# Kernel tuning notes

Measured on AMD Instinct MI355X. Metric: run time of the kernel, lower is better.

## Reference

```python
import jax, jax.numpy as jnp
import numpy as np

jax.config.update("jax_enable_x64", True)  # I-BERT's FixedPointMul runs in double precision

# I-BERT IntSoftmax constants
COEF0 = 0.35815147
COEF1 = 0.96963238 / COEF0
COEF2 = 1.0 / COEF0
X0 = -0.6931          # -ln(2)
N_EXP = 30            # large integer n in int_exp
MAX_BIT = 32
OUTPUT_BIT = 8
ACT_BIT = 16

B, H, S = 1, 12, 2048


def sg(x):
    return jax.lax.stop_gradient(x)


def ste_round(x):
    # straight-through round (matches torch round_ste / SymmetricQuantFunction backward)
    return x + sg(jnp.round(x) - x)


def ste_floor(x):
    return x + sg(jnp.floor(x) - x)


def sym_scale(x_min, x_max, bits):
    # symmetric_linear_quantization_params: scale = clamp(max(|min|,|max|),1e-8)/(2^(b-1)-1)
    n = 2 ** (bits - 1) - 1
    s = jnp.maximum(jnp.abs(x_min), jnp.abs(x_max))
    return sg(jnp.maximum(s, 1e-8) / n)


def fixedpoint_mul(pre_act, pre_sf, z_sf, bits):
    # I-BERT fixedpoint_mul: requantize pre_act (granularity pre_sf) to scale z_sf
    # using a 31-bit mantissa frexp decomposition, computed in float64.
    n = 2 ** (bits - 1) - 1
    z_int = ste_round(pre_act.astype(jnp.float64) / pre_sf.astype(jnp.float64))
    new_scale = sg((pre_sf / z_sf).astype(jnp.float64))
    e = jnp.floor(jnp.log2(jnp.abs(new_scale))) + 1.0   # frexp exponent
    m_int = jnp.round((new_scale / 2.0 ** e) * 2.0 ** 31)  # 31-bit mantissa
    out = ste_round(z_int * m_int / 2.0 ** (31.0 - e))
    return jnp.clip(out, -n - 1, n).astype(jnp.float32)


def quant_softmax(x):
    n16 = 2 ** (ACT_BIT - 1) - 1
    # ---- outer QuantAct(16, symmetric), specified min/max = data min/max ----
    sf = sym_scale(sg(x.min()), sg(x.max()), ACT_BIT)
    x_int = jnp.clip(ste_round(x / sf), -n16 - 1, n16)
    quant_x = x_int * sf  # dequantized activation returned by QuantAct
    # ---- IntSoftmax ----
    xi = quant_x / sf
    xi = xi - xi.max(axis=-1, keepdims=True)
    # int_exp: shift-based exponential, exp(x) = 2^(-q) * exp(r), r in (-ln2, 0]
    x0_int = sg(jnp.floor(X0 / sf))               # negative integer
    xi = jnp.maximum(xi, N_EXP * x0_int)
    q = ste_floor(xi / x0_int)
    r = xi - x0_int * q
    # int_polynomial: 2nd-order poly approximation of exp on (-ln2, 0]
    b_int = sg(jnp.floor(COEF1 / sf))
    c_int = sg(jnp.floor(COEF2 / sf ** 2))
    z = r * (r + b_int) + c_int
    exp_sf = sg(COEF0 * sf ** 2) / 2.0 ** N_EXP
    exp_int = jnp.maximum(ste_floor(z * 2.0 ** (N_EXP - q)), 0.0)
    # ---- inner QuantAct(16): requantize exp to 16 bits to avoid overflow ----
    act_sf = sym_scale(sg(exp_int.min()), sg(exp_int.max()), ACT_BIT)
    exp_int16 = fixedpoint_mul(exp_int, exp_sf, act_sf, ACT_BIT)
    # ---- integer normalization to output_bit fixed point ----
    s = exp_int16.sum(axis=-1, keepdims=True)
    factor = ste_floor(2.0 ** MAX_BIT / s)
    out_int = ste_floor(exp_int16 * factor / 2.0 ** (MAX_BIT - OUTPUT_BIT))
    out_sf = 1.0 / 2.0 ** OUTPUT_BIT
    return out_int * out_sf  # softmax probs quantized to 1/256 grid


def setup_inputs() -> dict:
    key = jax.random.key(0)
    x = jax.random.normal(key, (B, H, S, S), dtype=jnp.float32)
    return {"x": x}


def reference(x):
    return quant_softmax(x)
```

## Files before the change

### kernel.cpp

```cpp
#include <hip/hip_runtime.h>
#include <math.h>


#define ROW_S 2048
#define MM_BLOCKS 2048

typedef float floatx4 __attribute__((ext_vector_type(4)));

struct Scalars {
    double exp_sf_d;
    double inv_exp_sf;
    double m_int;
    double inv_pow;
    float  sf;
    float  inv_sf;
    float  x0_int;
    float  inv_x0;
    float  b_int;
    float  c_int;
    float  thirty_x0;
    float  _pad;
};

__device__ __forceinline__ float div_rn(float a, float b, float inv) {
    const float q0 = __fmul_rn(a, inv);
    const float r  = __fmaf_rn(-b, q0, a);
    return __fmaf_rn(r, inv, q0);
}
__device__ __forceinline__ double ddiv_rn(double a, double b, double inv) {
    const double q0 = __dmul_rn(a, inv);
    const double r  = __fma_rn(-b, q0, a);
    return __fma_rn(r, inv, q0);
}

__global__ __launch_bounds__(256) void k_minmax(const float* __restrict__ x,
                                                float* __restrict__ pmin,
                                                float* __restrict__ pmax,
                                                int n4) {
    const int tid = threadIdx.x;
    float vmin = INFINITY, vmax = -INFINITY;
    const float4* x4 = (const float4*)x;
    for (int i = blockIdx.x * 256 + tid; i < n4; i += MM_BLOCKS * 256) {
        float4 v = x4[i];
        vmin = fminf(vmin, fminf(fminf(v.x, v.y), fminf(v.z, v.w)));
        vmax = fmaxf(vmax, fmaxf(fmaxf(v.x, v.y), fmaxf(v.z, v.w)));
    }
#pragma unroll
    for (int m = 32; m > 0; m >>= 1) {
        vmin = fminf(vmin, __shfl_xor(vmin, m));
        vmax = fmaxf(vmax, __shfl_xor(vmax, m));
    }
    __shared__ float smin[4], smax[4];
    const int wave = tid >> 6, lane = tid & 63;
    if (lane == 0) { smin[wave] = vmin; smax[wave] = vmax; }
    __syncthreads();
    if (tid == 0) {
        pmin[blockIdx.x] = fminf(fminf(smin[0], smin[1]), fminf(smin[2], smin[3]));
        pmax[blockIdx.x] = fmaxf(fmaxf(smax[0], smax[1]), fmaxf(smax[2], smax[3]));
    }
}

__global__ __launch_bounds__(256) void k_scalars(const float* __restrict__ pmin,
                                                 const float* __restrict__ pmax,
                                                 Scalars* __restrict__ sc) {
    const int tid = threadIdx.x;
    float vmin = INFINITY, vmax = -INFINITY;
    for (int i = tid; i < MM_BLOCKS; i += 256) {
        vmin = fminf(vmin, pmin[i]);
        vmax = fmaxf(vmax, pmax[i]);
    }
#pragma unroll
    for (int m = 32; m > 0; m >>= 1) {
        vmin = fminf(vmin, __shfl_xor(vmin, m));
        vmax = fmaxf(vmax, __shfl_xor(vmax, m));
    }
    __shared__ float smin[4], smax[4];
    const int wave = tid >> 6, lane = tid & 63;
    if (lane == 0) { smin[wave] = vmin; smax[wave] = vmax; }
    __syncthreads();
    if (tid == 0) {
        const float xmin = fminf(fminf(smin[0], smin[1]), fminf(smin[2], smin[3]));
        const float xmax = fmaxf(fmaxf(smax[0], smax[1]), fmaxf(smax[2], smax[3]));
        const float sabs  = fmaxf(fabsf(xmin), fabsf(xmax));
        const float sf    = __fdiv_rn(fmaxf(sabs, 1e-8f), 32767.0f);
        const float x0i   = floorf(__fdiv_rn((float)(-0.6931), sf));
        const float sfsq  = __fmul_rn(sf, sf);
        const float b_int = floorf(__fdiv_rn((float)(0.96963238 / 0.35815147), sf));
        const float c_int = floorf(__fdiv_rn((float)(1.0 / 0.35815147), sfsq));
        const float exp_sf = __fdiv_rn(__fmul_rn((float)(0.35815147), sfsq), 1073741824.0f);
        const float emax   = __fmul_rn(c_int, 1073741824.0f);
        const float act_sf = __fdiv_rn(fmaxf(emax, 1e-8f), 32767.0f);
        const float  nsf = __fdiv_rn(exp_sf, act_sf);
        const double ns  = (double)nsf;
        int E;
        (void)frexp(ns, &E);
        const double m_int = rint(ldexp(ns, 31 - E));
        sc->exp_sf_d   = (double)exp_sf;
        sc->inv_exp_sf = 1.0 / (double)exp_sf;
        sc->m_int      = m_int;
        sc->inv_pow    = ldexp(1.0, E - 31);
        sc->sf         = sf;
        sc->inv_sf     = __fdiv_rn(1.0f, sf);
        sc->x0_int     = x0i;
        sc->inv_x0     = __fdiv_rn(1.0f, x0i);
        sc->b_int      = b_int;
        sc->c_int      = c_int;
        sc->thirty_x0  = __fmul_rn(30.0f, x0i);
    }
}

__global__ __launch_bounds__(256) void k_row(const float* __restrict__ x,
                                             float* __restrict__ out,
                                             const Scalars* __restrict__ scp) {
    const int tid = threadIdx.x;
    const size_t rowbase = (size_t)blockIdx.x * ROW_S;
    const float4* x4 = (const float4*)(x + rowbase);
    floatx4* o4 = (floatx4*)(out + rowbase);

    const float4 va = x4[tid];
    const float4 vb = x4[tid + 256];

    const Scalars sc = *scp;
    const float sf = sc.sf, inv_sf = sc.inv_sf;

    float xv[8] = {va.x, va.y, va.z, va.w, vb.x, vb.y, vb.z, vb.w};

    float xi[8];
    float vmax = -INFINITY;
#pragma unroll
    for (int j = 0; j < 8; ++j) {
        float t = rintf(div_rn(xv[j], sf, inv_sf));
        t = fminf(fmaxf(t, -32768.0f), 32767.0f);
        t = __fmul_rn(t, sf);
        t = div_rn(t, sf, inv_sf);
        xi[j] = t;
        vmax = fmaxf(vmax, t);
    }

    __shared__ float red[8];
    const int wave = tid >> 6, lane = tid & 63;
#pragma unroll
    for (int m = 32; m > 0; m >>= 1) vmax = fmaxf(vmax, __shfl_xor(vmax, m));
    if (lane == 0) red[wave] = vmax;
    __syncthreads();
    const float ximax = fmaxf(fmaxf(red[0], red[1]), fmaxf(red[2], red[3]));

    float e16[8];
    float ssum = 0.0f;
#pragma unroll
    for (int j = 0; j < 8; ++j) {
        const float xs = __fsub_rn(xi[j], ximax);
        const float xm = fmaxf(xs, sc.thirty_x0);
        const float qf = floorf(div_rn(xm, sc.x0_int, sc.inv_x0));
        const float r  = __fsub_rn(xm, __fmul_rn(sc.x0_int, qf));
        const float z  = __fadd_rn(__fmul_rn(r, __fadd_rn(r, sc.b_int)), sc.c_int);
        const int   qi = (int)qf;
        const float p2 = __int_as_float((157 - qi) << 23);
        const float ei = fmaxf(floorf(__fmul_rn(z, p2)), 0.0f);
        const double a  = (double)ei;
        const double zi = rint(ddiv_rn(a, sc.exp_sf_d, sc.inv_exp_sf));
        double ov = rint(__dmul_rn(__dmul_rn(zi, sc.m_int), sc.inv_pow));
        ov = fmin(fmax(ov, -32768.0), 32767.0);
        const float v = (float)ov;
        e16[j] = v;
        ssum += v;
    }

#pragma unroll
    for (int m = 32; m > 0; m >>= 1) ssum += __shfl_xor(ssum, m);
    if (lane == 0) red[4 + wave] = ssum;
    __syncthreads();
    const float s = ((red[4] + red[5]) + (red[6] + red[7]));
    const float factor = floorf(__fdiv_rn(4294967296.0f, s));

    float ov[8];
#pragma unroll
    for (int j = 0; j < 8; ++j) {
        const float oi = floorf(__fmul_rn(__fmul_rn(e16[j], factor), 5.9604644775390625e-8f));
        ov[j] = __fmul_rn(oi, 0.00390625f);
    }
    floatx4 w0 = {ov[0], ov[1], ov[2], ov[3]};
    floatx4 w1 = {ov[4], ov[5], ov[6], ov[7]};
    __builtin_nontemporal_store(w0, &o4[tid]);
    __builtin_nontemporal_store(w1, &o4[tid + 256]);
}

extern "C" void kernel_launch(void* const* d_in, const int* in_sizes, int n_in,
                              void* d_out, int out_size, void* d_ws, size_t ws_size,
                              hipStream_t stream) {
    const float* x = (const float*)d_in[0];
    float* out = (float*)d_out;
    const int n = in_sizes[0];
    const int rows = n / ROW_S;

    Scalars* sc = (Scalars*)d_ws;
    float* pmin = (float*)((char*)d_ws + 256);
    float* pmax = pmin + MM_BLOCKS;

    k_minmax<<<MM_BLOCKS, 256, 0, stream>>>(x, pmin, pmax, n / 4);
    k_scalars<<<1, 256, 0, stream>>>(pmin, pmax, sc);
    k_row<<<rows, 256, 0, stream>>>(x, out, sc);
}
```

Before: 355.7 us.

## Fuse scalar computation into amax kernel and process one row per wave

Replaces the min/max pass and the separate single-block scalar kernel with one abs-max kernel. It combines block results through an atomicMax on float bits, and the last block, found with an atomic counter, computes the quantization scalars. The row kernel now assigns one row per wavefront, so the row max and sum are taken with shuffles only and the shared-memory barriers disappear. The row max is taken on raw x and quantized afterwards, since the quantization is monotonic, which saves per-element work before the max. It adds a memset launch and relies on atomics and a thread fence for ordering.

```diff
diff --git a/kernel.cpp b/kernel.cpp
--- a/kernel.cpp
+++ b/kernel.cpp
@@ -33,156 +33,132 @@
     return __fma_rn(r, inv, q0);
 }
 
-__global__ __launch_bounds__(256) void k_minmax(const float* __restrict__ x,
-                                                float* __restrict__ pmin,
-                                                float* __restrict__ pmax,
-                                                int n4) {
+__global__ __launch_bounds__(256) void k_amax(const float* __restrict__ x,
+                                              unsigned* __restrict__ amax_bits,
+                                              unsigned* __restrict__ counter,
+                                              Scalars* __restrict__ sc,
+                                              int n4) {
     const int tid = threadIdx.x;
-    float vmin = INFINITY, vmax = -INFINITY;
+    float am = 0.0f;
     const float4* x4 = (const float4*)x;
     for (int i = blockIdx.x * 256 + tid; i < n4; i += MM_BLOCKS * 256) {
         float4 v = x4[i];
-        vmin = fminf(vmin, fminf(fminf(v.x, v.y), fminf(v.z, v.w)));
-        vmax = fmaxf(vmax, fmaxf(fmaxf(v.x, v.y), fmaxf(v.z, v.w)));
+        am = fmaxf(am, fabsf(v.x));
+        am = fmaxf(am, fabsf(v.y));
+        am = fmaxf(am, fabsf(v.z));
+        am = fmaxf(am, fabsf(v.w));
     }
 #pragma unroll
-    for (int m = 32; m > 0; m >>= 1) {
-        vmin = fminf(vmin, __shfl_xor(vmin, m));
-        vmax = fmaxf(vmax, __shfl_xor(vmax, m));
-    }
-    __shared__ float smin[4], smax[4];
+    for (int m = 32; m > 0; m >>= 1) am = fmaxf(am, __shfl_xor(am, m));
+    __shared__ float sred[4];
     const int wave = tid >> 6, lane = tid & 63;
-    if (lane == 0) { smin[wave] = vmin; smax[wave] = vmax; }
+    if (lane == 0) sred[wave] = am;
     __syncthreads();
     if (tid == 0) {
-        pmin[blockIdx.x] = fminf(fminf(smin[0], smin[1]), fminf(smin[2], smin[3]));
-        pmax[blockIdx.x] = fmaxf(fmaxf(smax[0], smax[1]), fmaxf(smax[2], smax[3]));
-    }
-}
-
-__global__ __launch_bounds__(256) void k_scalars(const float* __restrict__ pmin,
-                                                 const float* __restrict__ pmax,
-                                                 Scalars* __restrict__ sc) {
-    const int tid = threadIdx.x;
-    float vmin = INFINITY, vmax = -INFINITY;
-    for (int i = tid; i < MM_BLOCKS; i += 256) {
-        vmin = fminf(vmin, pmin[i]);
-        vmax = fmaxf(vmax, pmax[i]);
-    }
-#pragma unroll
-    for (int m = 32; m > 0; m >>= 1) {
-        vmin = fminf(vmin, __shfl_xor(vmin, m));
-        vmax = fmaxf(vmax, __shfl_xor(vmax, m));
-    }
-    __shared__ float smin[4], smax[4];
-    const int wave = tid >> 6, lane = tid & 63;
-    if (lane == 0) { smin[wave] = vmin; smax[wave] = vmax; }
-    __syncthreads();
-    if (tid == 0) {
-        const float xmin = fminf(fminf(smin[0], smin[1]), fminf(smin[2], smin[3]));
-        const float xmax = fmaxf(fmaxf(smax[0], smax[1]), fmaxf(smax[2], smax[3]));
-        const float sabs  = fmaxf(fabsf(xmin), fabsf(xmax));
-        const float sf    = __fdiv_rn(fmaxf(sabs, 1e-8f), 32767.0f);
-        const float x0i   = floorf(__fdiv_rn((float)(-0.6931), sf));
-        const float sfsq  = __fmul_rn(sf, sf);
-        const float b_int = floorf(__fdiv_rn((float)(0.96963238 / 0.35815147), sf));
-        const float c_int = floorf(__fdiv_rn((float)(1.0 / 0.35815147), sfsq));
-        const float exp_sf = __fdiv_rn(__fmul_rn((float)(0.35815147), sfsq), 1073741824.0f);
-        const float emax   = __fmul_rn(c_int, 1073741824.0f);
-        const float act_sf = __fdiv_rn(fmaxf(emax, 1e-8f), 32767.0f);
-        const float  nsf = __fdiv_rn(exp_sf, act_sf);
-        const double ns  = (double)nsf;
-        int E;
-        (void)frexp(ns, &E);
-        const double m_int = rint(ldexp(ns, 31 - E));
-        sc->exp_sf_d   = (double)exp_sf;
-        sc->inv_exp_sf = 1.0 / (double)exp_sf;
-        sc->m_int      = m_int;
-        sc->inv_pow    = ldexp(1.0, E - 31);
-        sc->sf         = sf;
-        sc->inv_sf     = __fdiv_rn(1.0f, sf);
-        sc->x0_int     = x0i;
-        sc->inv_x0     = __fdiv_rn(1.0f, x0i);
-        sc->b_int      = b_int;
-        sc->c_int      = c_int;
-        sc->thirty_x0  = __fmul_rn(30.0f, x0i);
+        const float ba = fmaxf(fmaxf(sred[0], sred[1]), fmaxf(sred[2], sred[3]));
+        atomicMax(amax_bits, __float_as_uint(ba));
+        __threadfence();
+        const unsigned old = atomicAdd(counter, 1u);
+        if (old == MM_BLOCKS - 1) {
+            const float sabs = __uint_as_float(atomicMax(amax_bits, 0u));
+            const float sf    = __fdiv_rn(fmaxf(sabs, 1e-8f), 32767.0f);
+            const float x0i   = floorf(__fdiv_rn((float)(-0.6931), sf));
+            const float sfsq  = __fmul_rn(sf, sf);
+            const float b_int = floorf(__fdiv_rn((float)(0.96963238 / 0.35815147), sf));
+            const float c_int = floorf(__fdiv_rn((float)(1.0 / 0.35815147), sfsq));
+            const float exp_sf = __fdiv_rn(__fmul_rn((float)(0.35815147), sfsq), 1073741824.0f);
+            const float emax   = __fmul_rn(c_int, 1073741824.0f);
+            const float act_sf = __fdiv_rn(fmaxf(emax, 1e-8f), 32767.0f);
+            const float  nsf = __fdiv_rn(exp_sf, act_sf);
+            const double ns  = (double)nsf;
+            int E;
+            (void)frexp(ns, &E);
+            const double m_int = rint(ldexp(ns, 31 - E));
+            sc->exp_sf_d   = (double)exp_sf;
+            sc->inv_exp_sf = 1.0 / (double)exp_sf;
+            sc->m_int      = m_int;
+            sc->inv_pow    = ldexp(1.0, E - 31);
+            sc->sf         = sf;
+            sc->inv_sf     = __fdiv_rn(1.0f, sf);
+            sc->x0_int     = x0i;
+            sc->inv_x0     = __fdiv_rn(1.0f, x0i);
+            sc->b_int      = b_int;
+            sc->c_int      = c_int;
+            sc->thirty_x0  = __fmul_rn(30.0f, x0i);
+        }
     }
 }
 
 __global__ __launch_bounds__(256) void k_row(const float* __restrict__ x,
                                              float* __restrict__ out,
                                              const Scalars* __restrict__ scp) {
-    const int tid = threadIdx.x;
-    const size_t rowbase = (size_t)blockIdx.x * ROW_S;
-    const float4* x4 = (const float4*)(x + rowbase);
-    floatx4* o4 = (floatx4*)(out + rowbase);
+    const int lane = threadIdx.x & 63;
+    const int wave = threadIdx.x >> 6;
+    const size_t row = (size_t)blockIdx.x * 4 + wave;
+    const floatx4* x4 = (const floatx4*)(x + row * ROW_S);
+    floatx4* o4 = (floatx4*)(out + row * ROW_S);
 
-    const float4 va = x4[tid];
-    const float4 vb = x4[tid + 256];
+    floatx4 v[8];
+#pragma unroll
+    for (int i = 0; i < 8; ++i) v[i] = x4[i * 64 + lane];
 
     const Scalars sc = *scp;
     const float sf = sc.sf, inv_sf = sc.inv_sf;
 
-    float xv[8] = {va.x, va.y, va.z, va.w, vb.x, vb.y, vb.z, vb.w};
+    float rmax = -INFINITY;
+#pragma unroll
+    for (int i = 0; i < 8; ++i) {
+#pragma unroll
+        for (int c = 0; c < 4; ++c) rmax = fmaxf(rmax, v[i][c]);
+    }
+#pragma unroll
+    for (int m = 32; m > 0; m >>= 1) rmax = fmaxf(rmax, __shfl_xor(rmax, m));
 
-    float xi[8];
-    float vmax = -INFINITY;
-#pragma unroll
-    for (int j = 0; j < 8; ++j) {
-        float t = rintf(div_rn(xv[j], sf, inv_sf));
-        t = fminf(fmaxf(t, -32768.0f), 32767.0f);
-        t = __fmul_rn(t, sf);
-        t = div_rn(t, sf, inv_sf);
-        xi[j] = t;
-        vmax = fmaxf(vmax, t);
-    }
+    float t = rintf(div_rn(rmax, sf, inv_sf));
+    t = fminf(fmaxf(t, -32768.0f), 32767.0f);
+    t = __fmul_rn(t, sf);
+    const float ximax = div_rn(t, sf, inv_sf);
 
-    __shared__ float red[8];
-    const int wave = tid >> 6, lane = tid & 63;
-#pragma unroll
-    for (int m = 32; m > 0; m >>= 1) vmax = fmaxf(vmax, __shfl_xor(vmax, m));
-    if (lane == 0) red[wave] = vmax;
-    __syncthreads();
-    const float ximax = fmaxf(fmaxf(red[0], red[1]), fmaxf(red[2], red[3]));
-
-    float e16[8];
     float ssum = 0.0f;
 #pragma unroll
-    for (int j = 0; j < 8; ++j) {
-        const float xs = __fsub_rn(xi[j], ximax);
-        const float xm = fmaxf(xs, sc.thirty_x0);
-        const float qf = floorf(div_rn(xm, sc.x0_int, sc.inv_x0));
-        const float r  = __fsub_rn(xm, __fmul_rn(sc.x0_int, qf));
-        const float z  = __fadd_rn(__fmul_rn(r, __fadd_rn(r, sc.b_int)), sc.c_int);
-        const int   qi = (int)qf;
-        const float p2 = __int_as_float((157 - qi) << 23);
-        const float ei = fmaxf(floorf(__fmul_rn(z, p2)), 0.0f);
-        const double a  = (double)ei;
-        const double zi = rint(ddiv_rn(a, sc.exp_sf_d, sc.inv_exp_sf));
-        double ov = rint(__dmul_rn(__dmul_rn(zi, sc.m_int), sc.inv_pow));
-        ov = fmin(fmax(ov, -32768.0), 32767.0);
-        const float v = (float)ov;
-        e16[j] = v;
-        ssum += v;
+    for (int i = 0; i < 8; ++i) {
+#pragma unroll
+        for (int c = 0; c < 4; ++c) {
+            float q = rintf(div_rn(v[i][c], sf, inv_sf));
+            q = fminf(fmaxf(q, -32768.0f), 32767.0f);
+            q = __fmul_rn(q, sf);
+            const float xi = div_rn(q, sf, inv_sf);
+            const float xs = __fsub_rn(xi, ximax);
+            const float xm = fmaxf(xs, sc.thirty_x0);
+            const float qf = floorf(div_rn(xm, sc.x0_int, sc.inv_x0));
+            const float r  = __fsub_rn(xm, __fmul_rn(sc.x0_int, qf));
+            const float z  = __fadd_rn(__fmul_rn(r, __fadd_rn(r, sc.b_int)), sc.c_int);
+            const int   qi = (int)qf;
+            const float p2 = __int_as_float((157 - qi) << 23);
+            const float ei = fmaxf(floorf(__fmul_rn(z, p2)), 0.0f);
+            const double a  = (double)ei;
+            const double zi = rint(ddiv_rn(a, sc.exp_sf_d, sc.inv_exp_sf));
+            double ovd = rint(__dmul_rn(__dmul_rn(zi, sc.m_int), sc.inv_pow));
+            ovd = fmin(fmax(ovd, -32768.0), 32767.0);
+            const float e16 = (float)ovd;
+            v[i][c] = e16;
+            ssum += e16;
+        }
     }
+#pragma unroll
+    for (int m = 32; m > 0; m >>= 1) ssum += __shfl_xor(ssum, m);
+    const float factor = floorf(__fdiv_rn(4294967296.0f, ssum));
 
 #pragma unroll
-    for (int m = 32; m > 0; m >>= 1) ssum += __shfl_xor(ssum, m);
-    if (lane == 0) red[4 + wave] = ssum;
-    __syncthreads();
-    const float s = ((red[4] + red[5]) + (red[6] + red[7]));
-    const float factor = floorf(__fdiv_rn(4294967296.0f, s));
-
-    float ov[8];
+    for (int i = 0; i < 8; ++i) {
+        floatx4 w;
 #pragma unroll
-    for (int j = 0; j < 8; ++j) {
-        const float oi = floorf(__fmul_rn(__fmul_rn(e16[j], factor), 5.9604644775390625e-8f));
-        ov[j] = __fmul_rn(oi, 0.00390625f);
+        for (int c = 0; c < 4; ++c) {
+            const float oi = floorf(__fmul_rn(__fmul_rn(v[i][c], factor), 5.9604644775390625e-8f));
+            w[c] = __fmul_rn(oi, 0.00390625f);
+        }
+        __builtin_nontemporal_store(w, &o4[i * 64 + lane]);
     }
-    floatx4 w0 = {ov[0], ov[1], ov[2], ov[3]};
-    floatx4 w1 = {ov[4], ov[5], ov[6], ov[7]};
-    __builtin_nontemporal_store(w0, &o4[tid]);
-    __builtin_nontemporal_store(w1, &o4[tid + 256]);
 }
 
 extern "C" void kernel_launch(void* const* d_in, const int* in_sizes, int n_in,
@@ -193,11 +169,11 @@
     const int n = in_sizes[0];
     const int rows = n / ROW_S;
 
-    Scalars* sc = (Scalars*)d_ws;
-    float* pmin = (float*)((char*)d_ws + 256);
-    float* pmax = pmin + MM_BLOCKS;
+    unsigned* amax_bits = (unsigned*)d_ws;
+    unsigned* counter   = amax_bits + 1;
+    Scalars*  sc        = (Scalars*)((char*)d_ws + 64);
 
-    k_minmax<<<MM_BLOCKS, 256, 0, stream>>>(x, pmin, pmax, n / 4);
-    k_scalars<<<1, 256, 0, stream>>>(pmin, pmax, sc);
-    k_row<<<rows, 256, 0, stream>>>(x, out, sc);
+    hipMemsetAsync(d_ws, 0, 8, stream);
+    k_amax<<<MM_BLOCKS, 256, 0, stream>>>(x, amax_bits, counter, sc, n / 4);
+    k_row<<<rows / 4, 256, 0, stream>>>(x, out, sc);
 }
```

New measurement: 408.7 us. 1.15x slower.
